# Kernel tuning notes

Measured on AMD Instinct MI355X. Metric: run time of the kernel, lower is better.

The kernel has to match this reference:

```python
import jax, jax.numpy as jnp
import numpy as np

H_GRID, W_GRID = 32, 32
KH, KW = 7, 11
NUM_HEADS = 8


def local_window_mask(H, W, kh, kw):
    # Token (h,w) may attend to (h',w') iff |h-h'|<=kh//2 and |w-w'|<=kw//2
    # (equivalent to the padded/cropped construction in the torch module).
    hh = jnp.arange(H)
    ww = jnp.arange(W)
    ok_h = jnp.abs(hh[:, None] - hh[None, :]) <= kh // 2  # [H,H]
    ok_w = jnp.abs(ww[:, None] - ww[None, :]) <= kw // 2  # [W,W]
    ok = ok_h[:, None, :, None] & ok_w[None, :, None, :]  # [H,W,H,W]
    ok = ok.reshape(H * W, H * W)
    return jnp.where(ok, 0.0, -jnp.inf)[None, None]  # [1,1,N,N]


def setup_inputs() -> dict:
    key = jax.random.key(0)
    k1, k2, k3, k4, k5 = jax.random.split(key, 5)
    B, N, E = 8, H_GRID * W_GRID, 256
    return {
        "x": jax.random.normal(k1, (B, N, E), dtype=jnp.float32),
        "qkv_w": jax.random.normal(k2, (3 * E, E), dtype=jnp.float32) * 0.02,
        "qkv_b": jax.random.normal(k3, (3 * E,), dtype=jnp.float32) * 0.02,
        "proj_w": jax.random.normal(k4, (E, E), dtype=jnp.float32) * 0.02,
        "proj_b": jax.random.normal(k5, (E,), dtype=jnp.float32) * 0.02,
    }


def reference(x, qkv_w, qkv_b, proj_w, proj_b):
    B, N, E = x.shape
    dh = E // NUM_HEADS
    scale = E ** (-0.5)  # note: embed_dim scaling, as in the original module
    qkv = x @ qkv_w.T + qkv_b                       # [B,N,3E]
    qkv = qkv.reshape(B, N, 3, NUM_HEADS, dh).transpose(2, 0, 3, 1, 4)
    q, k, v = qkv[0] * scale, qkv[1], qkv[2]        # [B,H,N,dh]
    attn = jnp.einsum('bhnd,bhmd->bhnm', q, k)      # [B,H,N,N]
    attn = attn + local_window_mask(H_GRID, W_GRID, KH, KW)
    attn = jax.nn.softmax(attn, axis=-1)
    out = jnp.einsum('bhnm,bhmd->bhnd', attn, v)    # [B,H,N,dh]
    out = out.transpose(0, 2, 1, 3).reshape(B, N, E)
    return out @ proj_w.T + proj_b
```

## Files before the change

kernel.cpp:

```cpp
#include <hip/hip_runtime.h>
#include <math.h>

constexpr int Bb = 8;
constexpr int Ns = 1024;
constexpr int Es = 256;
constexpr int NH = 8;
constexpr int DH = 32;
constexpr int Mrows = Bb * Ns;

constexpr int NX = Mrows * Es;
constexpr int NQ = 3 * Es * Es;
constexpr int NP = Es * Es;

typedef __bf16 bf16x8 __attribute__((ext_vector_type(8)));
typedef float  f32x4  __attribute__((ext_vector_type(4)));
union U4B8 { uint4 u; bf16x8 b; };

__device__ __forceinline__ unsigned short f2bf(float f) {
    union { float f; unsigned u; } c; c.f = f;
    unsigned r = (c.u + 0x7FFFu + ((c.u >> 16) & 1u)) >> 16;
    return (unsigned short)r;
}
__device__ __forceinline__ float bf2f(unsigned short h) {
    union { unsigned u; float f; } c; c.u = ((unsigned)h) << 16;
    return c.f;
}

__global__ __launch_bounds__(256)
void cast_bf16(const float* __restrict__ x, const float* __restrict__ wq,
               const float* __restrict__ wp, unsigned short* __restrict__ xb,
               unsigned short* __restrict__ wqb, unsigned short* __restrict__ wpb)
{
    int i = (blockIdx.x * 256 + threadIdx.x) * 4;
    const float* src; unsigned short* dst;
    if (i < NX)            { src = x  + i;             dst = xb  + i; }
    else if (i < NX + NQ)  { src = wq + (i - NX);      dst = wqb + (i - NX); }
    else                   { src = wp + (i - NX - NQ); dst = wpb + (i - NX - NQ); }
    float4 f = *(const float4*)src;
    ushort4 u;
    u.x = f2bf(f.x); u.y = f2bf(f.y); u.z = f2bf(f.z); u.w = f2bf(f.w);
    *(ushort4*)dst = u;
}

#define GLD 72

template<int MODE>
__global__ __launch_bounds__(256)
void gemm_mfma(const unsigned short* __restrict__ A, const unsigned short* __restrict__ W,
               const float* __restrict__ bias,
               unsigned short* __restrict__ qo, unsigned short* __restrict__ ko,
               unsigned short* __restrict__ vto, float* __restrict__ fo)
{
    __shared__ unsigned short As[64 * GLD];
    __shared__ unsigned short Ws[64 * GLD];

    const int t = threadIdx.x;
    const int m0 = blockIdx.x * 64;
    const int j0 = blockIdx.y * 64;

    const int srow = t >> 2;
    const int scol = (t & 3) * 16;

    const int lane = t & 63;
    const int wave = t >> 6;
    const int wm = (wave & 1) * 32;
    const int wn = (wave >> 1) * 32;
    const int fm = lane & 15;
    const int fq = lane >> 4;

    f32x4 acc[2][2];
    #pragma unroll
    for (int i = 0; i < 2; i++)
        #pragma unroll
        for (int j = 0; j < 2; j++)
            acc[i][j] = (f32x4){0.f, 0.f, 0.f, 0.f};

    for (int k0 = 0; k0 < Es; k0 += 64) {
        const uint4 a0 = *(const uint4*)(A + (size_t)(m0 + srow) * Es + k0 + scol);
        const uint4 a1 = *(const uint4*)(A + (size_t)(m0 + srow) * Es + k0 + scol + 8);
        const uint4 w0 = *(const uint4*)(W + (size_t)(j0 + srow) * Es + k0 + scol);
        const uint4 w1 = *(const uint4*)(W + (size_t)(j0 + srow) * Es + k0 + scol + 8);
        __syncthreads();
        *(uint4*)&As[srow * GLD + scol] = a0;
        *(uint4*)&As[srow * GLD + scol + 8] = a1;
        *(uint4*)&Ws[srow * GLD + scol] = w0;
        *(uint4*)&Ws[srow * GLD + scol + 8] = w1;
        __syncthreads();
        #pragma unroll
        for (int ks = 0; ks < 64; ks += 32) {
            U4B8 af0, af1, bf0, bf1;
            af0.u = *(const uint4*)&As[(wm +      fm) * GLD + ks + fq * 8];
            af1.u = *(const uint4*)&As[(wm + 16 + fm) * GLD + ks + fq * 8];
            bf0.u = *(const uint4*)&Ws[(wn +      fm) * GLD + ks + fq * 8];
            bf1.u = *(const uint4*)&Ws[(wn + 16 + fm) * GLD + ks + fq * 8];
            acc[0][0] = __builtin_amdgcn_mfma_f32_16x16x32_bf16(af0.b, bf0.b, acc[0][0], 0, 0, 0);
            acc[0][1] = __builtin_amdgcn_mfma_f32_16x16x32_bf16(af0.b, bf1.b, acc[0][1], 0, 0, 0);
            acc[1][0] = __builtin_amdgcn_mfma_f32_16x16x32_bf16(af1.b, bf0.b, acc[1][0], 0, 0, 0);
            acc[1][1] = __builtin_amdgcn_mfma_f32_16x16x32_bf16(af1.b, bf1.b, acc[1][1], 0, 0, 0);
        }
    }

    #pragma unroll
    for (int mt = 0; mt < 2; mt++) {
        #pragma unroll
        for (int nt = 0; nt < 2; nt++) {
            #pragma unroll
            for (int r = 0; r < 4; r++) {
                int row = m0 + wm + mt * 16 + fq * 4 + r;
                int col = j0 + wn + nt * 16 + fm;
                float val = acc[mt][nt][r] + bias[col];
                if (MODE == 0) {
                    int part = col >> 8;
                    int head = (col >> 5) & 7;
                    int d = col & 31;
                    int b = row >> 10;
                    int n = row & 1023;
                    int bh = b * NH + head;
                    if (part == 0)
                        qo[((size_t)bh * Ns + n) * DH + d] = f2bf(val * 0.0625f);
                    else if (part == 1)
                        ko[((size_t)bh * Ns + n) * DH + d] = f2bf(val);
                    else
                        vto[((size_t)bh * DH + d) * Ns + n] = f2bf(val);
                } else {
                    fo[(size_t)row * Es + col] = val;
                }
            }
        }
    }
}

#define SST 228
#define PST 232

__global__ __launch_bounds__(256)
void attn_mfma(const unsigned short* __restrict__ qb, const unsigned short* __restrict__ kb,
               const unsigned short* __restrict__ vtb, unsigned short* __restrict__ aob)
{
    __shared__ float S[32 * SST];
    __shared__ unsigned short Pb[32 * PST];
    __shared__ float Linv[32];

    const int blk = blockIdx.x;
    const int hq  = blk & 31;
    const int bh  = blk >> 5;
    const int t   = threadIdx.x;
    const int lane = t & 63;
    const int w    = t >> 6;
    const int fm = lane & 15;
    const int fq = lane >> 4;

    int n0c = (hq - 3) * 32;
    n0c = n0c < 0 ? 0 : (n0c > Ns - 224 ? Ns - 224 : n0c);

    const int qbase = (w & 1) * 16;
    const int sel   = w >> 1;
    const int dbase = (w >> 1) * 16;

    const unsigned short* vrow = vtb + ((size_t)bh * DH + dbase + fm) * Ns;
    uint4 vpre[7];
    #pragma unroll
    for (int i = 0; i < 7; i++)
        vpre[i] = *(const uint4*)(vrow + n0c + i * 32 + fq * 8);

    U4B8 qa;
    qa.u = *(const uint4*)(qb + ((size_t)bh * Ns + hq * 32 + qbase + fm) * DH + fq * 8);

    #pragma unroll
    for (int i = 0; i < 7; i++) {
        int kt = sel + 2 * i;
        U4B8 kf;
        kf.u = *(const uint4*)(kb + ((size_t)bh * Ns + n0c + kt * 16 + fm) * DH + fq * 8);
        f32x4 s = __builtin_amdgcn_mfma_f32_16x16x32_bf16(qa.b, kf.b, (f32x4){0.f,0.f,0.f,0.f}, 0, 0, 0);
        #pragma unroll
        for (int r = 0; r < 4; r++)
            S[(qbase + fq * 4 + r) * SST + kt * 16 + fm] = s[r];
    }
    __syncthreads();

    const int sq = t >> 3;
    const int l8 = t & 7;
    float sv[28];
    float smax = -INFINITY;
    #pragma unroll
    for (int i = 0; i < 28; i++) {
        int j = l8 + 8 * i;
        int g = n0c + j;
        int gh = g >> 5, gw = g & 31;
        int dh_ = gh - hq, dw_ = gw - sq;
        bool ok = (dh_ >= -3) && (dh_ <= 3) && (dw_ >= -5) && (dw_ <= 5);
        float x = ok ? S[sq * SST + j] : -INFINITY;
        sv[i] = x;
        smax = fmaxf(smax, x);
    }
    #pragma unroll
    for (int m = 1; m < 8; m <<= 1) smax = fmaxf(smax, __shfl_xor(smax, m));

    float lsum = 0.f;
    #pragma unroll
    for (int i = 0; i < 28; i++) {
        float p = __expf(sv[i] - smax);
        unsigned short pu = f2bf(p);
        Pb[sq * PST + l8 + 8 * i] = pu;
        lsum += bf2f(pu);
    }
    #pragma unroll
    for (int m = 1; m < 8; m <<= 1) lsum += __shfl_xor(lsum, m);
    if (l8 == 0) Linv[sq] = 1.f / lsum;
    __syncthreads();

    f32x4 acc = (f32x4){0.f, 0.f, 0.f, 0.f};
    #pragma unroll
    for (int i = 0; i < 7; i++) {
        U4B8 pa, vb;
        pa.u = *(const uint4*)&Pb[(qbase + fm) * PST + i * 32 + fq * 8];
        vb.u = vpre[i];
        acc = __builtin_amdgcn_mfma_f32_16x16x32_bf16(pa.b, vb.b, acc, 0, 0, 0);
    }

    const int b = bh >> 3, h = bh & 7;
    #pragma unroll
    for (int r = 0; r < 4; r++) {
        int qq = qbase + fq * 4 + r;
        float o = acc[r] * Linv[qq];
        aob[((size_t)(b * Ns) + hq * 32 + qq) * Es + h * DH + dbase + fm] = f2bf(o);
    }
}

extern "C" void kernel_launch(void* const* d_in, const int* in_sizes, int n_in,
                              void* d_out, int out_size, void* d_ws, size_t ws_size,
                              hipStream_t stream) {
    const float* x      = (const float*)d_in[0];
    const float* qkv_w  = (const float*)d_in[1];
    const float* qkv_b  = (const float*)d_in[2];
    const float* proj_w = (const float*)d_in[3];
    const float* proj_b = (const float*)d_in[4];
    float* out = (float*)d_out;

    unsigned short* xb  = (unsigned short*)d_ws;
    unsigned short* wqb = xb + NX;
    unsigned short* wpb = wqb + NQ;
    unsigned short* qb  = wpb + NP;
    unsigned short* kb  = qb + NX;
    unsigned short* vtb = kb + NX;
    unsigned short* aob = vtb + NX;

    dim3 blk(256);

    cast_bf16<<<dim3((NX + NQ + NP) / 4 / 256), blk, 0, stream>>>(x, qkv_w, proj_w, xb, wqb, wpb);

    dim3 g_qkv(Mrows / 64, (3 * Es) / 64);
    gemm_mfma<0><<<g_qkv, blk, 0, stream>>>(xb, wqb, qkv_b, qb, kb, vtb, nullptr);

    dim3 g_att(Bb * NH * 32);
    attn_mfma<<<g_att, blk, 0, stream>>>(qb, kb, vtb, aob);

    dim3 g_prj(Mrows / 64, Es / 64);
    gemm_mfma<1><<<g_prj, blk, 0, stream>>>(aob, wpb, proj_b, nullptr, nullptr, nullptr, out);
}
```

Before: 103.9 us.

## Fuse cast, QKV GEMM, attention and projection into one persistent kernel with grid barriers

Replaces four kernel launches with a single persistent kernel of 512 blocks. Inside it, the QKV GEMM, windowed attention and output projection phases are separated by atomic-based grid barriers. The separate bf16 cast pass is removed: the GEMM tiles now load fp32 and convert to bf16 while staging into shared memory. The attention output is kept in fp32 and converted inside the projection GEMM. This is meant to cut launch overhead and the extra cast round-trip through memory. In exchange it relies on all 512 blocks being co-resident for the barrier to be safe, doubles the attention-output traffic, and redoes the weight conversion in every tile.

```diff
diff --git a/kernel.cpp b/kernel.cpp
--- a/kernel.cpp
+++ b/kernel.cpp
@@ -7,14 +7,13 @@
 constexpr int NH = 8;
 constexpr int DH = 32;
 constexpr int Mrows = Bb * Ns;
-
 constexpr int NX = Mrows * Es;
-constexpr int NQ = 3 * Es * Es;
-constexpr int NP = Es * Es;
+
+#define NBLK 512
 
 typedef __bf16 bf16x8 __attribute__((ext_vector_type(8)));
 typedef float  f32x4  __attribute__((ext_vector_type(4)));
-union U4B8 { uint4 u; bf16x8 b; };
+union U4B8 { uint4 u; bf16x8 b; unsigned short s[8]; };
 
 __device__ __forceinline__ unsigned short f2bf(float f) {
     union { float f; unsigned u; } c; c.f = f;
@@ -26,38 +25,37 @@
     return c.f;
 }
 
-__global__ __launch_bounds__(256)
-void cast_bf16(const float* __restrict__ x, const float* __restrict__ wq,
-               const float* __restrict__ wp, unsigned short* __restrict__ xb,
-               unsigned short* __restrict__ wqb, unsigned short* __restrict__ wpb)
+__device__ __forceinline__ void grid_barrier(unsigned* cnt, unsigned* gen) {
+    __syncthreads();
+    if (threadIdx.x == 0) {
+        __threadfence();
+        unsigned g = atomicAdd(gen, 0u);
+        unsigned a = atomicAdd(cnt, 1u);
+        if (a == NBLK - 1) {
+            atomicExch(cnt, 0u);
+            atomicAdd(gen, 1u);
+        } else {
+            while (atomicAdd(gen, 0u) == g) { __builtin_amdgcn_s_sleep(2); }
+        }
+        __threadfence();
+    }
+    __syncthreads();
+}
+
+#define GLD 72
+#define SST 228
+#define PST 232
+#define SMEM_BYTES 44288
+
+template<int MODE>
+__device__ __forceinline__
+void gemm_tile(const float* __restrict__ A, const float* __restrict__ W,
+               const float* __restrict__ bias, int m0, int j0,
+               unsigned short* As, unsigned short* Ws,
+               unsigned short* qo, unsigned short* ko, unsigned short* vto,
+               float* fo)
 {
-    int i = (blockIdx.x * 256 + threadIdx.x) * 4;
-    const float* src; unsigned short* dst;
-    if (i < NX)            { src = x  + i;             dst = xb  + i; }
-    else if (i < NX + NQ)  { src = wq + (i - NX);      dst = wqb + (i - NX); }
-    else                   { src = wp + (i - NX - NQ); dst = wpb + (i - NX - NQ); }
-    float4 f = *(const float4*)src;
-    ushort4 u;
-    u.x = f2bf(f.x); u.y = f2bf(f.y); u.z = f2bf(f.z); u.w = f2bf(f.w);
-    *(ushort4*)dst = u;
-}
-
-#define GLD 72
-
-template<int MODE>
-__global__ __launch_bounds__(256)
-void gemm_mfma(const unsigned short* __restrict__ A, const unsigned short* __restrict__ W,
-               const float* __restrict__ bias,
-               unsigned short* __restrict__ qo, unsigned short* __restrict__ ko,
-               unsigned short* __restrict__ vto, float* __restrict__ fo)
-{
-    __shared__ unsigned short As[64 * GLD];
-    __shared__ unsigned short Ws[64 * GLD];
-
     const int t = threadIdx.x;
-    const int m0 = blockIdx.x * 64;
-    const int j0 = blockIdx.y * 64;
-
     const int srow = t >> 2;
     const int scol = (t & 3) * 16;
 
@@ -75,16 +73,33 @@
         for (int j = 0; j < 2; j++)
             acc[i][j] = (f32x4){0.f, 0.f, 0.f, 0.f};
 
+    const float* Arow = A + (size_t)(m0 + srow) * Es;
+    const float* Wrow = W + (size_t)(j0 + srow) * Es;
+
     for (int k0 = 0; k0 < Es; k0 += 64) {
-        const uint4 a0 = *(const uint4*)(A + (size_t)(m0 + srow) * Es + k0 + scol);
-        const uint4 a1 = *(const uint4*)(A + (size_t)(m0 + srow) * Es + k0 + scol + 8);
-        const uint4 w0 = *(const uint4*)(W + (size_t)(j0 + srow) * Es + k0 + scol);
-        const uint4 w1 = *(const uint4*)(W + (size_t)(j0 + srow) * Es + k0 + scol + 8);
+        float4 av[4], wv[4];
+        #pragma unroll
+        for (int i = 0; i < 4; i++) {
+            av[i] = *(const float4*)(Arow + k0 + scol + 4 * i);
+            wv[i] = *(const float4*)(Wrow + k0 + scol + 4 * i);
+        }
+        U4B8 pa0, pa1, pw0, pw1;
+        #pragma unroll
+        for (int i = 0; i < 2; i++) {
+            pa0.s[4*i+0] = f2bf(av[i].x); pa0.s[4*i+1] = f2bf(av[i].y);
+            pa0.s[4*i+2] = f2bf(av[i].z); pa0.s[4*i+3] = f2bf(av[i].w);
+            pa1.s[4*i+0] = f2bf(av[i+2].x); pa1.s[4*i+1] = f2bf(av[i+2].y);
+            pa1.s[4*i+2] = f2bf(av[i+2].z); pa1.s[4*i+3] = f2bf(av[i+2].w);
+            pw0.s[4*i+0] = f2bf(wv[i].x); pw0.s[4*i+1] = f2bf(wv[i].y);
+            pw0.s[4*i+2] = f2bf(wv[i].z); pw0.s[4*i+3] = f2bf(wv[i].w);
+            pw1.s[4*i+0] = f2bf(wv[i+2].x); pw1.s[4*i+1] = f2bf(wv[i+2].y);
+            pw1.s[4*i+2] = f2bf(wv[i+2].z); pw1.s[4*i+3] = f2bf(wv[i+2].w);
+        }
         __syncthreads();
-        *(uint4*)&As[srow * GLD + scol] = a0;
-        *(uint4*)&As[srow * GLD + scol + 8] = a1;
-        *(uint4*)&Ws[srow * GLD + scol] = w0;
-        *(uint4*)&Ws[srow * GLD + scol + 8] = w1;
+        *(uint4*)&As[srow * GLD + scol]     = pa0.u;
+        *(uint4*)&As[srow * GLD + scol + 8] = pa1.u;
+        *(uint4*)&Ws[srow * GLD + scol]     = pw0.u;
+        *(uint4*)&Ws[srow * GLD + scol + 8] = pw1.u;
         __syncthreads();
         #pragma unroll
         for (int ks = 0; ks < 64; ks += 32) {
@@ -99,6 +114,7 @@
             acc[1][1] = __builtin_amdgcn_mfma_f32_16x16x32_bf16(af1.b, bf1.b, acc[1][1], 0, 0, 0);
         }
     }
+    __syncthreads();
 
     #pragma unroll
     for (int mt = 0; mt < 2; mt++) {
@@ -130,21 +146,12 @@
     }
 }
 
-#define SST 228
-#define PST 232
-
-__global__ __launch_bounds__(256)
-void attn_mfma(const unsigned short* __restrict__ qb, const unsigned short* __restrict__ kb,
-               const unsigned short* __restrict__ vtb, unsigned short* __restrict__ aob)
+__device__ __forceinline__
+void attn_unit(const unsigned short* __restrict__ qb, const unsigned short* __restrict__ kb,
+               const unsigned short* __restrict__ vtb, float* __restrict__ aob,
+               int bh, int hq, float* S, unsigned short* Pb, float* Linv)
 {
-    __shared__ float S[32 * SST];
-    __shared__ unsigned short Pb[32 * PST];
-    __shared__ float Linv[32];
-
-    const int blk = blockIdx.x;
-    const int hq  = blk & 31;
-    const int bh  = blk >> 5;
-    const int t   = threadIdx.x;
+    const int t = threadIdx.x;
     const int lane = t & 63;
     const int w    = t >> 6;
     const int fm = lane & 15;
@@ -222,9 +229,43 @@
     #pragma unroll
     for (int r = 0; r < 4; r++) {
         int qq = qbase + fq * 4 + r;
-        float o = acc[r] * Linv[qq];
-        aob[((size_t)(b * Ns) + hq * 32 + qq) * Es + h * DH + dbase + fm] = f2bf(o);
-    }
+        aob[((size_t)(b * Ns) + hq * 32 + qq) * Es + h * DH + dbase + fm] = acc[r] * Linv[qq];
+    }
+    __syncthreads();
+}
+
+__global__ __launch_bounds__(256, 2)
+void fused_wattn(const float* __restrict__ x, const float* __restrict__ qkv_w,
+                 const float* __restrict__ qkv_b, const float* __restrict__ proj_w,
+                 const float* __restrict__ proj_b,
+                 unsigned short* __restrict__ qb, unsigned short* __restrict__ kb,
+                 unsigned short* __restrict__ vtb, float* __restrict__ aob,
+                 float* __restrict__ out, unsigned* __restrict__ bar)
+{
+    __shared__ __align__(16) char smem[SMEM_BYTES];
+    unsigned short* As = (unsigned short*)smem;
+    unsigned short* Ws = As + 64 * GLD;
+    float* S  = (float*)smem;
+    unsigned short* Pb = (unsigned short*)(smem + 29184);
+    float* Linv = (float*)(smem + 44032);
+
+    unsigned* cnt = bar;
+    unsigned* gen = bar + 1;
+
+    for (int u = blockIdx.x; u < 1536; u += NBLK)
+        gemm_tile<0>(x, qkv_w, qkv_b, (u & 127) * 64, (u >> 7) * 64,
+                     As, Ws, qb, kb, vtb, nullptr);
+
+    grid_barrier(cnt, gen);
+
+    for (int u = blockIdx.x; u < 2048; u += NBLK)
+        attn_unit(qb, kb, vtb, aob, u >> 5, u & 31, S, Pb, Linv);
+
+    grid_barrier(cnt, gen);
+
+    for (int u = blockIdx.x; u < 512; u += NBLK)
+        gemm_tile<1>(aob, proj_w, proj_b, (u & 127) * 64, (u >> 7) * 64,
+                     As, Ws, nullptr, nullptr, nullptr, out);
 }
 
 extern "C" void kernel_launch(void* const* d_in, const int* in_sizes, int n_in,
@@ -237,24 +278,13 @@
     const float* proj_b = (const float*)d_in[4];
     float* out = (float*)d_out;
 
-    unsigned short* xb  = (unsigned short*)d_ws;
-    unsigned short* wqb = xb + NX;
-    unsigned short* wpb = wqb + NQ;
-    unsigned short* qb  = wpb + NP;
+    unsigned* bar = (unsigned*)d_ws;
+    unsigned short* qb  = (unsigned short*)((char*)d_ws + 256);
     unsigned short* kb  = qb + NX;
     unsigned short* vtb = kb + NX;
-    unsigned short* aob = vtb + NX;
-
-    dim3 blk(256);
-
-    cast_bf16<<<dim3((NX + NQ + NP) / 4 / 256), blk, 0, stream>>>(x, qkv_w, proj_w, xb, wqb, wpb);
-
-    dim3 g_qkv(Mrows / 64, (3 * Es) / 64);
-    gemm_mfma<0><<<g_qkv, blk, 0, stream>>>(xb, wqb, qkv_b, qb, kb, vtb, nullptr);
-
-    dim3 g_att(Bb * NH * 32);
-    attn_mfma<<<g_att, blk, 0, stream>>>(qb, kb, vtb, aob);
-
-    dim3 g_prj(Mrows / 64, Es / 64);
-    gemm_mfma<1><<<g_prj, blk, 0, stream>>>(aob, wpb, proj_b, nullptr, nullptr, nullptr, out);
-}
+    float* aob = (float*)(vtb + NX);
+
+    hipMemsetAsync(d_ws, 0, 256, stream);
+    fused_wattn<<<dim3(NBLK), dim3(256), 0, stream>>>(
+        x, qkv_w, qkv_b, proj_w, proj_b, qb, kb, vtb, aob, out, bar);
+}
```

After: 220.3 us. 112% more time.
